# Kernel optimization log

Measured on AMD Instinct MI355X. Metric: run time of the kernel, lower is better.

Reference implementation:

```python
import jax, jax.numpy as jnp
import numpy as np
from jax import lax

NUM_SCALES = 3
BASE_WEIGHT = 1.0
BOUNDARY_WEIGHT = 2.0


def _avg_pool3d_same(x, k):
    # F.avg_pool3d(kernel=k, stride=1, padding=k//2, count_include_pad=True)
    # -> window sum with zero padding, divided by constant k**3.
    p = k // 2
    s = lax.reduce_window(
        x, jnp.array(0.0, x.dtype), lax.add,
        window_dimensions=(1, 1, k, k, k),
        window_strides=(1, 1, 1, 1, 1),
        padding=((0, 0), (0, 0), (p, p), (p, p), (p, p)),
    )
    return s / jnp.array(k ** 3, x.dtype)


def setup_inputs() -> dict:
    key = jax.random.key(0)
    k1, k2 = jax.random.split(key)
    logits = jax.random.normal(k1, (2, 2, 96, 192, 192), dtype=jnp.float32)
    labels = jax.random.randint(k2, (2, 1, 96, 192, 192), 0, 2, dtype=jnp.int32)
    return {"logits": logits, "labels": labels}


def reference(logits, labels):
    B, C = logits.shape[0], logits.shape[1]
    labels_sq = labels[:, 0].astype(jnp.int32)              # (B,D,H,W)
    onehot = jax.nn.one_hot(labels_sq, C, dtype=jnp.float32, axis=1)  # (B,C,D,H,W)

    # multi-scale boundary weight map: sum_s sum_c |onehot - avgpool_k(onehot)|
    weight_map = jnp.zeros((B, 1) + logits.shape[2:], dtype=jnp.float32)
    for scale_idx in range(NUM_SCALES):
        k = 3 + 2 * scale_idx
        smoothed = _avg_pool3d_same(onehot, k)
        weight_map = weight_map + jnp.abs(onehot - smoothed).sum(axis=1, keepdims=True)
    w_max = weight_map.max()
    weight_map = jnp.where(w_max > 0, weight_map / w_max, weight_map)

    pixel_weights = BASE_WEIGHT + BOUNDARY_WEIGHT * weight_map[:, 0]  # (B,D,H,W)

    log_probs = jax.nn.log_softmax(logits, axis=1)          # (B,C,D,H,W)
    nll = -jnp.take_along_axis(log_probs, labels_sq[:, None].astype(jnp.int32), axis=1)[:, 0]
    return (nll * pixel_weights).mean()
```

## Files before the change

### kernel.cpp

```cpp
#include <hip/hip_runtime.h>

#define BB 2
#define CC 2
#define DD 96
#define HH 192
#define WW 192
static constexpr int NV   = BB * DD * HH * WW;
static constexpr int HW_  = HH * WW;
static constexpr int DHW_ = DD * HW_;
static constexpr int ROWS = BB * DD * HH;
static constexpr int QPR  = WW / 4;

static constexpr int SEGQ = 8;
static constexpr int NSEG = QPR / SEGQ;
static constexpr int LSTR = SEGQ + 1;
static constexpr int WHBLKS = BB * DD * NSEG;

static constexpr int LBLKS = ROWS / 16;

#define K3 42875
#define K5 9261
#define K7 3375

#define PM1  0x00010001u
#define PM3  0x00030003u
#define PM7  0x00070007u
#define PMF  0x000F000Fu
#define PM1F 0x001F001Fu
#define PM3F 0x003F003Fu

__device__ __forceinline__ unsigned ypack(const unsigned* g) {
    unsigned t3 = ((g[2] >> 1) & PM3) + ((g[3] >> 1) & PM3) + ((g[4] >> 1) & PM3);
    unsigned t5 = ((g[1] >> 3) & PM7) + ((g[2] >> 3) & PM7) + ((g[3] >> 3) & PM7)
                + ((g[4] >> 3) & PM7) + ((g[5] >> 3) & PM7);
    unsigned t7 = ((g[0] >> 6) & PM7) + ((g[1] >> 6) & PM7) + ((g[2] >> 6) & PM7)
                + ((g[3] >> 6) & PM7) + ((g[4] >> 6) & PM7) + ((g[5] >> 6) & PM7)
                + ((g[6] >> 6) & PM7);
    return (g[3] & PM1) | (t3 << 1) | (t5 << 5) | (t7 << 10);
}

__global__ __launch_bounds__(256) void k_wh(const int* __restrict__ lab,
                                            unsigned short* __restrict__ ys) {
    __shared__ uint2 lds[HH * LSTR];
    int blk  = blockIdx.x;
    int seg  = blk % NSEG;
    int bd   = blk / NSEG;
    int base = bd * HW_;
    const int4* l4 = (const int4*)lab;
    int bq = base >> 2;

    for (int t = threadIdx.x; t < HH * SEGQ; t += 256) {
        int row  = t >> 3;
        int qloc = t & 7;
        int gq   = seg * SEGQ + qloc;
        int qi   = bq + row * QPR + gq;
        int4 cur = l4[qi];
        int4 prv = (gq > 0)       ? l4[qi - 1] : int4{0, 0, 0, 0};
        int4 nxt = (gq < QPR - 1) ? l4[qi + 1] : int4{0, 0, 0, 0};
        int v[12] = {prv.x, prv.y, prv.z, prv.w,
                     cur.x, cur.y, cur.z, cur.w,
                     nxt.x, nxt.y, nxt.z, nxt.w};
        int s7[4], s5[4], s3[4];
        s7[0] = v[1] + v[2] + v[3] + v[4] + v[5] + v[6] + v[7];
#pragma unroll
        for (int j = 0; j < 3; ++j) s7[j + 1] = s7[j] - v[j + 1] + v[j + 8];
#pragma unroll
        for (int j = 0; j < 4; ++j) {
            s5[j] = s7[j] - v[j + 1] - v[j + 7];
            s3[j] = s5[j] - v[j + 2] - v[j + 6];
        }
        unsigned o0 = (unsigned)(v[4] | (s3[0] << 1) | (s5[0] << 3) | (s7[0] << 6));
        unsigned o1 = (unsigned)(v[5] | (s3[1] << 1) | (s5[1] << 3) | (s7[1] << 6));
        unsigned o2 = (unsigned)(v[6] | (s3[2] << 1) | (s5[2] << 3) | (s7[2] << 6));
        unsigned o3 = (unsigned)(v[7] | (s3[3] << 1) | (s5[3] << 3) | (s7[3] << 6));
        uint2 st;
        st.x = o0 | (o1 << 16);
        st.y = o2 | (o3 << 16);
        lds[row * LSTR + qloc] = st;
    }
    __syncthreads();

    for (int t = threadIdx.x; t < HH * SEGQ; t += 256) {
        int row  = t >> 3;
        int qloc = t & 7;
        int gq   = seg * SEGQ + qloc;
        unsigned gx[7], gy[7];
#pragma unroll
        for (int k = 0; k < 7; ++k) {
            int hh = row + k - 3;
            if (hh >= 0 && hh < HH) {
                uint2 u = lds[hh * LSTR + qloc];
                gx[k] = u.x; gy[k] = u.y;
            } else { gx[k] = 0u; gy[k] = 0u; }
        }
        uint2 st;
        st.x = ypack(gx);
        st.y = ypack(gy);
        *(uint2*)(ys + base + row * WW + gq * 4) = st;
    }
}

__global__ __launch_bounds__(192) void k_loss(const unsigned short* __restrict__ ys,
                                              const float* __restrict__ logits,
                                              float* __restrict__ p_nll,
                                              float* __restrict__ p_nw,
                                              float* __restrict__ p_wm) {
    int tid  = threadIdx.x;
    int rloc = tid / 24;
    int q8   = tid % 24;
    bool interior = (q8 > 0) && (q8 < 23);

    float acc_n = 0.f, acc_p = 0.f, mx = 0.f;

#pragma unroll
    for (int it = 0; it < 2; ++it) {
        int row = blockIdx.x * 16 + it * 8 + rloc;
        int h   = row % HH;
        int rd  = row / HH;
        int d   = rd % DD;
        int b   = rd / DD;
        int i0  = row * WW + q8 * 8;

        unsigned u[7][4];
#pragma unroll
        for (int k = 0; k < 7; ++k) {
            int dd = d + k - 3;
            if (dd >= 0 && dd < DD) {
                uint4 t4 = *(const uint4*)(ys + i0 + (k - 3) * HW_);
                u[k][0] = t4.x; u[k][1] = t4.y; u[k][2] = t4.z; u[k][3] = t4.w;
            } else {
                u[k][0] = 0u; u[k][1] = 0u; u[k][2] = 0u; u[k][3] = 0u;
            }
        }
        unsigned S3[4], S5[4], S7[4];
#pragma unroll
        for (int w = 0; w < 4; ++w) {
            S3[w] = ((u[2][w] >> 1) & PMF) + ((u[3][w] >> 1) & PMF) + ((u[4][w] >> 1) & PMF);
            S5[w] = ((u[1][w] >> 5) & PM1F) + ((u[2][w] >> 5) & PM1F) + ((u[3][w] >> 5) & PM1F)
                  + ((u[4][w] >> 5) & PM1F) + ((u[5][w] >> 5) & PM1F);
            S7[w] = ((u[0][w] >> 10) & PM3F) + ((u[1][w] >> 10) & PM3F) + ((u[2][w] >> 10) & PM3F)
                  + ((u[3][w] >> 10) & PM3F) + ((u[4][w] >> 10) & PM3F) + ((u[5][w] >> 10) & PM3F)
                  + ((u[6][w] >> 10) & PM3F);
        }

        int ch3 = 1 + min(h, 1) + min(HH - 1 - h, 1);
        int ch5 = 1 + min(h, 2) + min(HH - 1 - h, 2);
        int ch7 = 1 + min(h, 3) + min(HH - 1 - h, 3);
        int cd3 = 1 + min(d, 1) + min(DD - 1 - d, 1);
        int cd5 = 1 + min(d, 2) + min(DD - 1 - d, 2);
        int cd7 = 1 + min(d, 3) + min(DD - 1 - d, 3);
        int A3 = ch3 * cd3 * K3;
        int B5 = ch5 * cd5 * K5;
        int C7 = ch7 * cd7 * K7;
        int inum = 3 * A3 + 5 * B5 + 7 * C7;

        const float* lp = logits + i0 + b * DHW_;
        const float4 A0 = *(const float4*)(lp);
        const float4 A1 = *(const float4*)(lp + 4);
        const float4 B0 = *(const float4*)(lp + DHW_);
        const float4 B1 = *(const float4*)(lp + DHW_ + 4);
        float l0[8] = {A0.x, A0.y, A0.z, A0.w, A1.x, A1.y, A1.z, A1.w};
        float l1[8] = {B0.x, B0.y, B0.z, B0.w, B1.x, B1.y, B1.z, B1.w};

#pragma unroll
        for (int j = 0; j < 8; ++j) {
            const int wd = j >> 1;
            const int sh = (j & 1) * 16;
            int S3j  = (int)((S3[wd] >> sh) & 0xFFFFu);
            int S5j  = (int)((S5[wd] >> sh) & 0xFFFFu);
            int S7j  = (int)((S7[wd] >> sh) & 0xFFFFu);
            int labj = (int)((u[3][wd] >> sh) & 1u);

            int Ssum = __mul24(S3j, K3) + __mul24(S5j, K5) + __mul24(S7j, K7);
            int cn = inum;
            if (!interior) {
                int w = q8 * 8 + j;
                int cw3 = 1 + min(w, 1) + min(WW - 1 - w, 1);
                int cw5 = 1 + min(w, 2) + min(WW - 1 - w, 2);
                int cw7 = 1 + min(w, 3) + min(WW - 1 - w, 3);
                cn = __mul24(cw3, A3) + __mul24(cw5, B5) + __mul24(cw7, C7);
            }
            float fq  = (float)(cn - 2 * Ssum) * (1.0f / 1157625.0f);
            float sgn = labj ? 1.0f : -1.0f;
            float wm  = fmaf(sgn, fq, 3.0f);
            float s   = sgn * (l0[j] - l1[j]);
            float nll = fmaxf(s, 0.f) + __logf(1.0f + __expf(-fabsf(s)));

            acc_n += nll;
            acc_p += nll * wm;
            mx = fmaxf(mx, wm);
        }
    }

#pragma unroll
    for (int off = 32; off > 0; off >>= 1) {
        acc_n += __shfl_down(acc_n, off);
        acc_p += __shfl_down(acc_p, off);
        mx     = fmaxf(mx, __shfl_down(mx, off));
    }
    __shared__ float s_n[3], s_p[3], s_m[3];
    int wid  = tid >> 6;
    int lane = tid & 63;
    if (lane == 0) { s_n[wid] = acc_n; s_p[wid] = acc_p; s_m[wid] = mx; }
    __syncthreads();
    if (tid == 0) {
        p_nll[blockIdx.x] = s_n[0] + s_n[1] + s_n[2];
        p_nw[blockIdx.x]  = s_p[0] + s_p[1] + s_p[2];
        p_wm[blockIdx.x]  = fmaxf(s_m[0], fmaxf(s_m[1], s_m[2]));
    }
}

__global__ __launch_bounds__(256) void k_fin(const float* __restrict__ pn,
                                             const float* __restrict__ pw,
                                             const float* __restrict__ pm,
                                             float* __restrict__ out) {
    double s = 0.0, p = 0.0;
    float mx = 0.f;
    for (int t = threadIdx.x; t < LBLKS; t += 256) {
        s += (double)pn[t];
        p += (double)pw[t];
        mx = fmaxf(mx, pm[t]);
    }
#pragma unroll
    for (int off = 32; off > 0; off >>= 1) {
        s  += __shfl_down(s, off);
        p  += __shfl_down(p, off);
        mx  = fmaxf(mx, __shfl_down(mx, off));
    }
    __shared__ double sh_s[4], sh_p[4];
    __shared__ float  sh_m[4];
    int wid  = threadIdx.x >> 6;
    int lane = threadIdx.x & 63;
    if (lane == 0) { sh_s[wid] = s; sh_p[wid] = p; sh_m[wid] = mx; }
    __syncthreads();
    if (threadIdx.x == 0) {
        double S = 0.0, P = 0.0;
        float  M = 0.f;
#pragma unroll
        for (int t = 0; t < 4; ++t) { S += sh_s[t]; P += sh_p[t]; M = fmaxf(M, sh_m[t]); }
        double res = (M > 0.f) ? (S + 2.0 * P / (double)M) : S;
        out[0] = (float)(res / (double)NV);
    }
}

extern "C" void kernel_launch(void* const* d_in, const int* in_sizes, int n_in,
                              void* d_out, int out_size, void* d_ws, size_t ws_size,
                              hipStream_t stream) {
    const float* logits = (const float*)d_in[0];
    const int*   labels = (const int*)d_in[1];
    float*       out    = (float*)d_out;

    char* ws = (char*)d_ws;
    float* p_nll = (float*)ws;
    float* p_nw  = (float*)(ws + 16384);
    float* p_wm  = (float*)(ws + 32768);
    unsigned short* ys = (unsigned short*)(ws + 65536);

    k_wh  <<<WHBLKS, 256, 0, stream>>>(labels, ys);
    k_loss<<<LBLKS, 192, 0, stream>>>(ys, logits, p_nll, p_nw, p_wm);
    k_fin <<<1, 256, 0, stream>>>(p_nll, p_nw, p_wm, out);
}
```

Measured before the change: 45.49 us.

## Stream k_loss along depth with register ring buffers for the D-direction window sums

The loss kernel now gives each thread a column of 4 voxels and walks 8 depth slices, keeping the shifted and masked packed-label fields for the last few slices in small register ring buffers. Each ys slice is then loaded once per thread instead of seven times, which cuts redundant global and L2 traffic in the depth-window reduction. In exchange the kernel uses more registers, loads only 8 bytes of ys and 16 bytes of logits per step instead of wider vectors, and reads 6 halo slices per chunk. The block count and the per-block partial layout change to match the new grid.

After: 45.01 us. Within noise of the previous version (-1.1%).

```diff
diff --git a/kernel.cpp b/kernel.cpp
--- a/kernel.cpp
+++ b/kernel.cpp
@@ -8,7 +8,6 @@
 static constexpr int NV   = BB * DD * HH * WW;
 static constexpr int HW_  = HH * WW;
 static constexpr int DHW_ = DD * HW_;
-static constexpr int ROWS = BB * DD * HH;
 static constexpr int QPR  = WW / 4;
 
 static constexpr int SEGQ = 8;
@@ -16,7 +15,12 @@
 static constexpr int LSTR = SEGQ + 1;
 static constexpr int WHBLKS = BB * DD * NSEG;
 
-static constexpr int LBLKS = ROWS / 16;
+static constexpr int W4   = 48;
+static constexpr int COLS = BB * HH * W4;
+static constexpr int DCH  = 8;
+static constexpr int NCH  = DD / DCH;
+static constexpr int CBLK = COLS / 256;
+static constexpr int LBLKS = CBLK * NCH;
 
 #define K3 42875
 #define K5 9261
@@ -27,6 +31,8 @@
 #define PM7  0x00070007u
 #define PMF  0x000F000Fu
 #define PM1F 0x001F001Fu
+#define PM3F 0x003F3F3Fu
+#undef  PM3F
 #define PM3F 0x003F003Fu
 
 __device__ __forceinline__ unsigned ypack(const unsigned* g) {
@@ -100,95 +106,103 @@
     }
 }
 
-__global__ __launch_bounds__(192) void k_loss(const unsigned short* __restrict__ ys,
+__global__ __launch_bounds__(256) void k_loss(const unsigned short* __restrict__ ys,
                                               const float* __restrict__ logits,
                                               float* __restrict__ p_nll,
                                               float* __restrict__ p_nw,
                                               float* __restrict__ p_wm) {
-    int tid  = threadIdx.x;
-    int rloc = tid / 24;
-    int q8   = tid % 24;
-    bool interior = (q8 > 0) && (q8 < 23);
-
+    int tid   = threadIdx.x;
+    int cb    = blockIdx.x % CBLK;
+    int chunk = blockIdx.x / CBLK;
+    int col   = cb * 256 + tid;
+    int w4    = col % W4;
+    int rowid = col / W4;
+    int h     = rowid % HH;
+    int b     = rowid / HH;
+    int d0    = chunk * DCH;
+    int w0    = w4 * 4;
+
+    int i_bh = b * DHW_ + h * WW + w0;
+    const float* lp = logits + i_bh + b * DHW_ + d0 * HW_;
+
+    int ch3 = 1 + min(h, 1) + min(HH - 1 - h, 1);
+    int ch5 = 1 + min(h, 2) + min(HH - 1 - h, 2);
+    int ch7 = 1 + min(h, 3) + min(HH - 1 - h, 3);
+    bool interior = (w4 > 0) && (w4 < W4 - 1);
+
+    unsigned e3[5][2], e5[6][2], e7[7][2], ur[4][2];
     float acc_n = 0.f, acc_p = 0.f, mx = 0.f;
 
 #pragma unroll
-    for (int it = 0; it < 2; ++it) {
-        int row = blockIdx.x * 16 + it * 8 + rloc;
-        int h   = row % HH;
-        int rd  = row / HH;
-        int d   = rd % DD;
-        int b   = rd / DD;
-        int i0  = row * WW + q8 * 8;
-
-        unsigned u[7][4];
-#pragma unroll
-        for (int k = 0; k < 7; ++k) {
-            int dd = d + k - 3;
-            if (dd >= 0 && dd < DD) {
-                uint4 t4 = *(const uint4*)(ys + i0 + (k - 3) * HW_);
-                u[k][0] = t4.x; u[k][1] = t4.y; u[k][2] = t4.z; u[k][3] = t4.w;
-            } else {
-                u[k][0] = 0u; u[k][1] = 0u; u[k][2] = 0u; u[k][3] = 0u;
+    for (int step = 0; step < DCH + 6; ++step) {
+        int ld = d0 - 3 + step;
+        uint2 t2 = {0u, 0u};
+        if (ld >= 0 && ld < DD)
+            t2 = *(const uint2*)(ys + i_bh + ld * HW_);
+        {
+            unsigned u0 = t2.x, u1 = t2.y;
+            ur[step % 4][0] = u0;                 ur[step % 4][1] = u1;
+            e3[step % 5][0] = (u0 >> 1) & PMF;    e3[step % 5][1] = (u1 >> 1) & PMF;
+            e5[step % 6][0] = (u0 >> 5) & PM1F;   e5[step % 6][1] = (u1 >> 5) & PM1F;
+            e7[step % 7][0] = (u0 >> 10) & PM3F;  e7[step % 7][1] = (u1 >> 10) & PM3F;
+        }
+        if (step >= 6) {
+            int dout = ld - 3;
+            unsigned S3w[2], S5w[2], S7w[2], lw[2];
+#pragma unroll
+            for (int wd = 0; wd < 2; ++wd) {
+                S3w[wd] = e3[(step - 4) % 5][wd] + e3[(step - 3) % 5][wd]
+                        + e3[(step - 2) % 5][wd];
+                S5w[wd] = e5[(step - 5) % 6][wd] + e5[(step - 4) % 6][wd]
+                        + e5[(step - 3) % 6][wd] + e5[(step - 2) % 6][wd]
+                        + e5[(step - 1) % 6][wd];
+                S7w[wd] = e7[(step - 6) % 7][wd] + e7[(step - 5) % 7][wd]
+                        + e7[(step - 4) % 7][wd] + e7[(step - 3) % 7][wd]
+                        + e7[(step - 2) % 7][wd] + e7[(step - 1) % 7][wd]
+                        + e7[(step - 0) % 7][wd];
+                lw[wd]  = ur[(step - 3) % 4][wd];
             }
-        }
-        unsigned S3[4], S5[4], S7[4];
-#pragma unroll
-        for (int w = 0; w < 4; ++w) {
-            S3[w] = ((u[2][w] >> 1) & PMF) + ((u[3][w] >> 1) & PMF) + ((u[4][w] >> 1) & PMF);
-            S5[w] = ((u[1][w] >> 5) & PM1F) + ((u[2][w] >> 5) & PM1F) + ((u[3][w] >> 5) & PM1F)
-                  + ((u[4][w] >> 5) & PM1F) + ((u[5][w] >> 5) & PM1F);
-            S7[w] = ((u[0][w] >> 10) & PM3F) + ((u[1][w] >> 10) & PM3F) + ((u[2][w] >> 10) & PM3F)
-                  + ((u[3][w] >> 10) & PM3F) + ((u[4][w] >> 10) & PM3F) + ((u[5][w] >> 10) & PM3F)
-                  + ((u[6][w] >> 10) & PM3F);
-        }
-
-        int ch3 = 1 + min(h, 1) + min(HH - 1 - h, 1);
-        int ch5 = 1 + min(h, 2) + min(HH - 1 - h, 2);
-        int ch7 = 1 + min(h, 3) + min(HH - 1 - h, 3);
-        int cd3 = 1 + min(d, 1) + min(DD - 1 - d, 1);
-        int cd5 = 1 + min(d, 2) + min(DD - 1 - d, 2);
-        int cd7 = 1 + min(d, 3) + min(DD - 1 - d, 3);
-        int A3 = ch3 * cd3 * K3;
-        int B5 = ch5 * cd5 * K5;
-        int C7 = ch7 * cd7 * K7;
-        int inum = 3 * A3 + 5 * B5 + 7 * C7;
-
-        const float* lp = logits + i0 + b * DHW_;
-        const float4 A0 = *(const float4*)(lp);
-        const float4 A1 = *(const float4*)(lp + 4);
-        const float4 B0 = *(const float4*)(lp + DHW_);
-        const float4 B1 = *(const float4*)(lp + DHW_ + 4);
-        float l0[8] = {A0.x, A0.y, A0.z, A0.w, A1.x, A1.y, A1.z, A1.w};
-        float l1[8] = {B0.x, B0.y, B0.z, B0.w, B1.x, B1.y, B1.z, B1.w};
-
-#pragma unroll
-        for (int j = 0; j < 8; ++j) {
-            const int wd = j >> 1;
-            const int sh = (j & 1) * 16;
-            int S3j  = (int)((S3[wd] >> sh) & 0xFFFFu);
-            int S5j  = (int)((S5[wd] >> sh) & 0xFFFFu);
-            int S7j  = (int)((S7[wd] >> sh) & 0xFFFFu);
-            int labj = (int)((u[3][wd] >> sh) & 1u);
-
-            int Ssum = __mul24(S3j, K3) + __mul24(S5j, K5) + __mul24(S7j, K7);
-            int cn = inum;
-            if (!interior) {
-                int w = q8 * 8 + j;
-                int cw3 = 1 + min(w, 1) + min(WW - 1 - w, 1);
-                int cw5 = 1 + min(w, 2) + min(WW - 1 - w, 2);
-                int cw7 = 1 + min(w, 3) + min(WW - 1 - w, 3);
-                cn = __mul24(cw3, A3) + __mul24(cw5, B5) + __mul24(cw7, C7);
+            int cd3 = 1 + min(dout, 1) + min(DD - 1 - dout, 1);
+            int cd5 = 1 + min(dout, 2) + min(DD - 1 - dout, 2);
+            int cd7 = 1 + min(dout, 3) + min(DD - 1 - dout, 3);
+            int A3 = ch3 * cd3 * K3;
+            int B5 = ch5 * cd5 * K5;
+            int C7 = ch7 * cd7 * K7;
+            int inum = 3 * A3 + 5 * B5 + 7 * C7;
+
+            const float4 L0 = *(const float4*)(lp + (step - 6) * HW_);
+            const float4 L1 = *(const float4*)(lp + (step - 6) * HW_ + DHW_);
+            float l0[4] = {L0.x, L0.y, L0.z, L0.w};
+            float l1[4] = {L1.x, L1.y, L1.z, L1.w};
+
+#pragma unroll
+            for (int j = 0; j < 4; ++j) {
+                const int wd = j >> 1;
+                const int sh = (j & 1) * 16;
+                int S3j  = (int)((S3w[wd] >> sh) & 0xFFFFu);
+                int S5j  = (int)((S5w[wd] >> sh) & 0xFFFFu);
+                int S7j  = (int)((S7w[wd] >> sh) & 0xFFFFu);
+                int labj = (int)((lw[wd] >> sh) & 1u);
+
+                int Ssum = __mul24(S3j, K3) + __mul24(S5j, K5) + __mul24(S7j, K7);
+                int cn = inum;
+                if (!interior) {
+                    int w = w0 + j;
+                    int cw3 = 1 + min(w, 1) + min(WW - 1 - w, 1);
+                    int cw5 = 1 + min(w, 2) + min(WW - 1 - w, 2);
+                    int cw7 = 1 + min(w, 3) + min(WW - 1 - w, 3);
+                    cn = __mul24(cw3, A3) + __mul24(cw5, B5) + __mul24(cw7, C7);
+                }
+                float fq  = (float)(cn - 2 * Ssum) * (1.0f / 1157625.0f);
+                float sgn = labj ? 1.0f : -1.0f;
+                float wm  = fmaf(sgn, fq, 3.0f);
+                float s   = sgn * (l0[j] - l1[j]);
+                float nll = fmaxf(s, 0.f) + __logf(1.0f + __expf(-fabsf(s)));
+
+                acc_n += nll;
+                acc_p += nll * wm;
+                mx = fmaxf(mx, wm);
             }
-            float fq  = (float)(cn - 2 * Ssum) * (1.0f / 1157625.0f);
-            float sgn = labj ? 1.0f : -1.0f;
-            float wm  = fmaf(sgn, fq, 3.0f);
-            float s   = sgn * (l0[j] - l1[j]);
-            float nll = fmaxf(s, 0.f) + __logf(1.0f + __expf(-fabsf(s)));
-
-            acc_n += nll;
-            acc_p += nll * wm;
-            mx = fmaxf(mx, wm);
         }
     }
 
@@ -198,15 +212,15 @@
         acc_p += __shfl_down(acc_p, off);
         mx     = fmaxf(mx, __shfl_down(mx, off));
     }
-    __shared__ float s_n[3], s_p[3], s_m[3];
+    __shared__ float s_n[4], s_p[4], s_m[4];
     int wid  = tid >> 6;
     int lane = tid & 63;
     if (lane == 0) { s_n[wid] = acc_n; s_p[wid] = acc_p; s_m[wid] = mx; }
     __syncthreads();
     if (tid == 0) {
-        p_nll[blockIdx.x] = s_n[0] + s_n[1] + s_n[2];
-        p_nw[blockIdx.x]  = s_p[0] + s_p[1] + s_p[2];
-        p_wm[blockIdx.x]  = fmaxf(s_m[0], fmaxf(s_m[1], s_m[2]));
+        p_nll[blockIdx.x] = s_n[0] + s_n[1] + s_n[2] + s_n[3];
+        p_nw[blockIdx.x]  = s_p[0] + s_p[1] + s_p[2] + s_p[3];
+        p_wm[blockIdx.x]  = fmaxf(fmaxf(s_m[0], s_m[1]), fmaxf(s_m[2], s_m[3]));
     }
 }
 
@@ -257,6 +271,6 @@
     unsigned short* ys = (unsigned short*)(ws + 65536);
 
     k_wh  <<<WHBLKS, 256, 0, stream>>>(labels, ys);
-    k_loss<<<LBLKS, 192, 0, stream>>>(ys, logits, p_nll, p_nw, p_wm);
+    k_loss<<<LBLKS, 256, 0, stream>>>(ys, logits, p_nll, p_nw, p_wm);
     k_fin <<<1, 256, 0, stream>>>(p_nll, p_nw, p_wm, out);
 }
```
